# Kernel tuning notes

Hardware: AMD Instinct MI355X
Metric: run time of the kernel (lower is better)

Reference implementation:

```python
import jax, jax.numpy as jnp
import numpy as np

N = 8192
IN_DIM = 512
OUT_DIM = 256
ALPHA = 0.2  # LeakyReLU negative slope


def setup_inputs() -> dict:
    key = jax.random.key(0)
    k_nodes, k_edge, k_W, k_Wb, k_a1, k_a1b, k_a2, k_a2b = jax.random.split(key, 8)
    nodes = jax.random.normal(k_nodes, (N, IN_DIM), dtype=jnp.float32)
    edge_mat = jax.random.uniform(k_edge, (N, N)) > 0.5
    edge_mat = edge_mat | jnp.eye(N, dtype=bool)
    s_W = 1.0 / np.sqrt(IN_DIM)
    s_a = 1.0 / np.sqrt(OUT_DIM)
    W_w = jax.random.uniform(k_W, (OUT_DIM, IN_DIM), minval=-s_W, maxval=s_W, dtype=jnp.float32)
    W_b = jax.random.uniform(k_Wb, (OUT_DIM,), minval=-s_W, maxval=s_W, dtype=jnp.float32)
    a1_w = jax.random.uniform(k_a1, (1, OUT_DIM), minval=-s_a, maxval=s_a, dtype=jnp.float32)
    a1_b = jax.random.uniform(k_a1b, (1,), minval=-s_a, maxval=s_a, dtype=jnp.float32)
    a2_w = jax.random.uniform(k_a2, (1, OUT_DIM), minval=-s_a, maxval=s_a, dtype=jnp.float32)
    a2_b = jax.random.uniform(k_a2b, (1,), minval=-s_a, maxval=s_a, dtype=jnp.float32)
    return {"nodes": nodes, "edge_mat": edge_mat, "W_w": W_w, "W_b": W_b,
            "a1_w": a1_w, "a1_b": a1_b, "a2_w": a2_w, "a2_b": a2_b}


def reference(nodes, edge_mat, W_w, W_b, a1_w, a1_b, a2_w, a2_b):
    Wh = nodes @ W_w.T + W_b                      # [N, OUT_DIM]
    Wh1 = Wh @ a1_w.T + a1_b                      # [N, 1]
    Wh2 = Wh @ a2_w.T + a2_b                      # [N, 1]
    scores = jax.nn.leaky_relu(Wh1 + Wh2.T, negative_slope=ALPHA)  # [N, N]
    masked = jnp.where(edge_mat, scores, -jnp.inf)
    attention = jax.nn.softmax(masked, axis=1)    # [N, N]
    return attention @ Wh                         # [N, OUT_DIM]
```

## Files before the change

kernel.cpp:

```cpp
#include <hip/hip_runtime.h>
#include <hip/hip_bf16.h>
#include <stdint.h>


#define NN 8192
#define IND 512
#define OUTD 256

typedef __attribute__((ext_vector_type(8))) short short8;
typedef __attribute__((ext_vector_type(4))) short short4v;
typedef __attribute__((ext_vector_type(4))) float f32x4;
typedef __attribute__((ext_vector_type(4))) int i32x4;

static __device__ __forceinline__ short f2bf(float f) {
  return __builtin_bit_cast(short, __float2bfloat16(f));
}

extern "C" __global__ __launch_bounds__(256) void k_convert_w(
    const float* __restrict__ W, short* __restrict__ W2) {
  const int t = blockIdx.x * 256 + threadIdx.x;
  const int row = t >> 6, kb = t & 63;
  const float* src = W + row * IND + kb * 8;
  f32x4 x0 = *(const f32x4*)src;
  f32x4 x1 = *(const f32x4*)(src + 4);
  short8 o;
  o[0] = f2bf(x0[0]); o[1] = f2bf(x0[1]); o[2] = f2bf(x0[2]); o[3] = f2bf(x0[3]);
  o[4] = f2bf(x1[0]); o[5] = f2bf(x1[1]); o[6] = f2bf(x1[2]); o[7] = f2bf(x1[3]);
  *(short8*)(W2 + (size_t)kb * 2048 + row * 8) = o;
}

extern "C" __global__ __launch_bounds__(128) void k_wh(
    const float* __restrict__ nodes, const short* __restrict__ W2,
    const float* __restrict__ Wb, const float* __restrict__ a1w,
    const float* __restrict__ a1b, const float* __restrict__ a2w,
    const float* __restrict__ a2b, short* __restrict__ WhL,
    float* __restrict__ s1, float* __restrict__ s2) {
  const int tid = threadIdx.x;
  const int wv = tid >> 6, lane = tid & 63, g = lane >> 4, m = lane & 15;
  const int rowbase = blockIdx.x * 32 + wv * 16;

  f32x4 acc[16];
#pragma unroll
  for (int nf = 0; nf < 16; ++nf) acc[nf] = (f32x4){0.f, 0.f, 0.f, 0.f};

  const float* arow = nodes + (size_t)(rowbase + m) * IND;
  const short* bb = W2 + (size_t)g * 2048 + m * 8;
#pragma unroll 4
  for (int k0 = 0; k0 < IND; k0 += 32) {
    const float* ap = arow + k0 + g * 8;
    f32x4 x0 = *(const f32x4*)ap;
    f32x4 x1 = *(const f32x4*)(ap + 4);
    short8 af;
    af[0] = f2bf(x0[0]); af[1] = f2bf(x0[1]); af[2] = f2bf(x0[2]); af[3] = f2bf(x0[3]);
    af[4] = f2bf(x1[0]); af[5] = f2bf(x1[1]); af[6] = f2bf(x1[2]); af[7] = f2bf(x1[3]);
    const short* bk = bb + (size_t)(k0 >> 3) * 2048;
#pragma unroll
    for (int nf = 0; nf < 16; ++nf) {
      short8 bf = *(const short8*)(bk + nf * 128);
      acc[nf] = __builtin_amdgcn_mfma_f32_16x16x32_bf16(af, bf, acc[nf], 0, 0, 0);
    }
  }

  float p1[4] = {0.f, 0.f, 0.f, 0.f}, p2[4] = {0.f, 0.f, 0.f, 0.f};
#pragma unroll
  for (int nf = 0; nf < 16; ++nf) {
    const int n = nf * 16 + m;
    const float b = Wb[n], c1 = a1w[n], c2 = a2w[n];
#pragma unroll
    for (int r = 0; r < 4; ++r) {
      float v = acc[nf][r] + b;
      acc[nf][r] = v;
      p1[r] += c1 * v;
      p2[r] += c2 * v;
    }
  }
#pragma unroll
  for (int off = 1; off < 16; off <<= 1) {
#pragma unroll
    for (int r = 0; r < 4; ++r) {
      p1[r] += __shfl_xor(p1[r], off);
      p2[r] += __shfl_xor(p2[r], off);
    }
  }
  if (m == 0) {
    const float b1 = a1b[0], b2 = a2b[0];
#pragma unroll
    for (int r = 0; r < 4; ++r) {
      const int row = rowbase + g * 4 + r;
      s1[row] = p1[r] + b1;
      s2[row] = p2[r] + b2;
    }
  }

  const size_t cbase = ((size_t)(rowbase >> 3) + (g >> 1)) * 2048 + (g & 1) * 4;
#pragma unroll
  for (int nf = 0; nf < 16; ++nf) {
    short4v o;
#pragma unroll
    for (int r = 0; r < 4; ++r) o[r] = f2bf(acc[nf][r]);
    *(short4v*)(WhL + cbase + (size_t)(nf * 16 + m) * 8) = o;
  }
}

extern "C" __global__ __launch_bounds__(512, 2) void k_attn(
    const int* __restrict__ mask, const short* __restrict__ WhL,
    const float* __restrict__ s1, const float* __restrict__ s2,
    float* __restrict__ out) {
  __shared__ f32x4 cbuf[3][64][32];
  __shared__ float denl[8][32];

  const int tid = threadIdx.x;
  const int w = tid >> 6, lane = tid & 63, g = lane >> 4, m = lane & 15;
  const int rg = blockIdx.x * 32;

  const float s1a = s1[rg + m];
  const float s1b = s1[rg + 16 + m];

  f32x4 acc0[16], acc1[16];
#pragma unroll
  for (int nf = 0; nf < 16; ++nf) {
    acc0[nf] = (f32x4){0.f, 0.f, 0.f, 0.f};
    acc1[nf] = (f32x4){0.f, 0.f, 0.f, 0.f};
  }
  float den0 = 0.f, den1 = 0.f;

  const int* mr0 = mask + (size_t)(rg + m) * NN + w * 1024 + g * 8;
  const int* mr1 = mr0 + (size_t)16 * NN;
  const float* sp = s2 + w * 1024 + g * 8;
  const short* bb = WhL + ((size_t)w * 128 + g) * 2048 + (size_t)m * 8;

  i32x4 ca0 = __builtin_nontemporal_load((const i32x4*)mr0);
  i32x4 ca1 = __builtin_nontemporal_load((const i32x4*)(mr0 + 4));
  i32x4 cb0 = __builtin_nontemporal_load((const i32x4*)mr1);
  i32x4 cb1 = __builtin_nontemporal_load((const i32x4*)(mr1 + 4));
  f32x4 cs0 = *(const f32x4*)sp;
  f32x4 cs1 = *(const f32x4*)(sp + 4);

  auto build = [&](float s1h, const i32x4& xlo, const i32x4& xhi,
                   const f32x4& slo, const f32x4& shi, float& den) -> short8 {
    short8 af;
#pragma unroll
    for (int i = 0; i < 4; ++i) {
      float sv = s1h + slo[i];
      sv = fmaxf(sv, 0.2f * sv);
      float pv = (xlo[i] != 0) ? __expf(sv) : 0.f;
      den += pv;
      af[i] = f2bf(pv);
    }
#pragma unroll
    for (int i = 0; i < 4; ++i) {
      float sv = s1h + shi[i];
      sv = fmaxf(sv, 0.2f * sv);
      float pv = (xhi[i] != 0) ? __expf(sv) : 0.f;
      den += pv;
      af[i + 4] = f2bf(pv);
    }
    return af;
  };

#pragma unroll 2
  for (int u = 0; u < 32; ++u) {
    const int un = (u < 31) ? (u + 1) : 31;
    i32x4 na0 = __builtin_nontemporal_load((const i32x4*)(mr0 + un * 32));
    i32x4 na1 = __builtin_nontemporal_load((const i32x4*)(mr0 + un * 32 + 4));
    i32x4 nb0 = __builtin_nontemporal_load((const i32x4*)(mr1 + un * 32));
    i32x4 nb1 = __builtin_nontemporal_load((const i32x4*)(mr1 + un * 32 + 4));
    f32x4 ns0 = *(const f32x4*)(sp + un * 32);
    f32x4 ns1 = *(const f32x4*)(sp + un * 32 + 4);

    short8 af0 = build(s1a, ca0, ca1, cs0, cs1, den0);
    short8 af1 = build(s1b, cb0, cb1, cs0, cs1, den1);

    const short* bu = bb + (size_t)u * 8192;
#pragma unroll
    for (int nf = 0; nf < 16; ++nf) {
      short8 bf = *(const short8*)(bu + nf * 128);
      acc0[nf] = __builtin_amdgcn_mfma_f32_16x16x32_bf16(af0, bf, acc0[nf], 0, 0, 0);
      acc1[nf] = __builtin_amdgcn_mfma_f32_16x16x32_bf16(af1, bf, acc1[nf], 0, 0, 0);
    }
    ca0 = na0; ca1 = na1; cb0 = nb0; cb1 = nb1; cs0 = ns0; cs1 = ns1;
  }

  den0 += __shfl_xor(den0, 16); den0 += __shfl_xor(den0, 32);
  den1 += __shfl_xor(den1, 16); den1 += __shfl_xor(den1, 32);
  if (lane < 16) { denl[w][m] = den0; denl[w][16 + m] = den1; }

  auto storeacc = [&](int b) {
#pragma unroll
    for (int nf = 0; nf < 16; ++nf) {
      cbuf[b][lane][nf ^ (lane & 7)] = acc0[nf];
      cbuf[b][lane][(16 + nf) ^ (lane & 7)] = acc1[nf];
    }
  };
  auto addacc = [&](int b) {
#pragma unroll
    for (int nf = 0; nf < 16; ++nf) {
      acc0[nf] += cbuf[b][lane][nf ^ (lane & 7)];
      acc1[nf] += cbuf[b][lane][(16 + nf) ^ (lane & 7)];
    }
  };

  __syncthreads();
  if (w >= 4 && w <= 6) storeacc(w - 4);
  __syncthreads();
  if (w < 3) addacc(w);
  __syncthreads();
  if (w == 7) storeacc(0);
  if (w == 3) storeacc(1);
  __syncthreads();
  if (w == 0) addacc(0);
  if (w == 1) addacc(1);
  __syncthreads();
  if (w == 1) storeacc(0);
  if (w == 2) storeacc(1);
  __syncthreads();
  if (w == 0) {
    addacc(0);
    addacc(1);
    float d0 = 0.f, d1 = 0.f;
#pragma unroll
    for (int ww = 0; ww < 8; ++ww) { d0 += denl[ww][m]; d1 += denl[ww][16 + m]; }
#pragma unroll
    for (int r = 0; r < 4; ++r) {
      const int q = g * 4 + r;
      const float i0 = 1.f / __shfl(d0, q);
      const float i1 = 1.f / __shfl(d1, q);
#pragma unroll
      for (int nf = 0; nf < 16; ++nf) {
        out[(size_t)(rg + q) * OUTD + nf * 16 + m] = acc0[nf][r] * i0;
        out[(size_t)(rg + 16 + q) * OUTD + nf * 16 + m] = acc1[nf][r] * i1;
      }
    }
  }
}

extern "C" void kernel_launch(void* const* d_in, const int* in_sizes, int n_in,
                              void* d_out, int out_size, void* d_ws, size_t ws_size,
                              hipStream_t stream) {
  const float* nodes = (const float*)d_in[0];
  const int*   mask  = (const int*)d_in[1];
  const float* W_w   = (const float*)d_in[2];
  const float* W_b   = (const float*)d_in[3];
  const float* a1w   = (const float*)d_in[4];
  const float* a1b   = (const float*)d_in[5];
  const float* a2w   = (const float*)d_in[6];
  const float* a2b   = (const float*)d_in[7];
  float* out = (float*)d_out;

  char* ws = (char*)d_ws;
  short* WhL = (short*)(ws);
  float* s1  = (float*)(ws + (size_t)4 * 1024 * 1024);
  float* s2  = (float*)(ws + (size_t)4 * 1024 * 1024 + 32768);
  short* W2  = (short*)(ws + (size_t)4 * 1024 * 1024 + 65536);

  hipLaunchKernelGGL(k_convert_w, dim3(64), dim3(256), 0, stream, W_w, W2);
  hipLaunchKernelGGL(k_wh, dim3(256), dim3(128), 0, stream,
                     nodes, W2, W_b, a1w, a1b, a2w, a2b, WhL, s1, s2);
  hipLaunchKernelGGL(k_attn, dim3(256), dim3(512), 0, stream,
                     mask, WhL, s1, s2, out);
}
```

Baseline: 178.0 us.

## Pack mask into bitmap and split attention over key chunks with combine pass

Adds a pre-pass that packs the int32 adjacency mask into a bitmap with wave ballots, so the attention kernel reads bits instead of full ints. The attention kernel is restructured so each block covers 128 rows and a quarter of the key range. Each wave holds 32 rows and 1024 keys, and two waves reduce per row group. Partial numerators and denominators go to workspace, and a new combine kernel sums them and normalizes. This raises per-block WhL reuse and cuts the cross-wave reduction, at the cost of two extra launches and an extra 32 MB partial write and read.

```diff
diff --git a/kernel.cpp b/kernel.cpp
--- a/kernel.cpp
+++ b/kernel.cpp
@@ -10,7 +10,6 @@
 typedef __attribute__((ext_vector_type(8))) short short8;
 typedef __attribute__((ext_vector_type(4))) short short4v;
 typedef __attribute__((ext_vector_type(4))) float f32x4;
-typedef __attribute__((ext_vector_type(4))) int i32x4;
 
 static __device__ __forceinline__ short f2bf(float f) {
   return __builtin_bit_cast(short, __float2bfloat16(f));
@@ -102,19 +101,44 @@
   }
 }
 
+extern "C" __global__ __launch_bounds__(256) void k_mask(
+    const int* __restrict__ mask, uint32_t* __restrict__ bm) {
+  const int tid = threadIdx.x;
+  const int wv = tid >> 6, lane = tid & 63;
+  const int gw = blockIdx.x * 4 + wv;
+  const size_t base = (size_t)gw * 16384;
+#pragma unroll 4
+  for (int it = 0; it < 64; ++it) {
+    const size_t ib = base + (size_t)it * 256;
+    unsigned long long b0 = __ballot(mask[ib + lane] != 0);
+    unsigned long long b1 = __ballot(mask[ib + 64 + lane] != 0);
+    unsigned long long b2 = __ballot(mask[ib + 128 + lane] != 0);
+    unsigned long long b3 = __ballot(mask[ib + 192 + lane] != 0);
+    if (lane < 8) {
+      unsigned long long s01 = (lane & 2) ? b1 : b0;
+      unsigned long long s23 = (lane & 2) ? b3 : b2;
+      unsigned long long sel = (lane & 4) ? s23 : s01;
+      bm[ib / 32 + lane] = (uint32_t)(sel >> ((lane & 1) * 32));
+    }
+  }
+}
+
 extern "C" __global__ __launch_bounds__(512, 2) void k_attn(
-    const int* __restrict__ mask, const short* __restrict__ WhL,
+    const uint32_t* __restrict__ bm, const short* __restrict__ WhL,
     const float* __restrict__ s1, const float* __restrict__ s2,
-    float* __restrict__ out) {
-  __shared__ f32x4 cbuf[3][64][32];
-  __shared__ float denl[8][32];
+    float* __restrict__ pnum, float* __restrict__ pden) {
+  __shared__ f32x4 cbuf[4][64][16];
+  __shared__ float dbuf[4][2][16];
 
   const int tid = threadIdx.x;
   const int w = tid >> 6, lane = tid & 63, g = lane >> 4, m = lane & 15;
-  const int rg = blockIdx.x * 32;
-
-  const float s1a = s1[rg + m];
-  const float s1b = s1[rg + 16 + m];
+  const int rt = blockIdx.x >> 2, jc = blockIdx.x & 3;
+  const int rg = w >> 1, js = w & 1;
+  const int rowbase = rt * 128 + rg * 32;
+  const int jbase = jc * 2048 + js * 1024;
+
+  const float s1a = s1[rowbase + m];
+  const float s1b = s1[rowbase + 16 + m];
 
   f32x4 acc0[16], acc1[16];
 #pragma unroll
@@ -124,36 +148,25 @@
   }
   float den0 = 0.f, den1 = 0.f;
 
-  const int* mr0 = mask + (size_t)(rg + m) * NN + w * 1024 + g * 8;
-  const int* mr1 = mr0 + (size_t)16 * NN;
-  const float* sp = s2 + w * 1024 + g * 8;
-  const short* bb = WhL + ((size_t)w * 128 + g) * 2048 + (size_t)m * 8;
-
-  i32x4 ca0 = __builtin_nontemporal_load((const i32x4*)mr0);
-  i32x4 ca1 = __builtin_nontemporal_load((const i32x4*)(mr0 + 4));
-  i32x4 cb0 = __builtin_nontemporal_load((const i32x4*)mr1);
-  i32x4 cb1 = __builtin_nontemporal_load((const i32x4*)(mr1 + 4));
+  const uint32_t* bw0 = bm + (size_t)(rowbase + m) * 256 + (jbase >> 5);
+  const uint32_t* bw1 = bw0 + (size_t)16 * 256;
+  const float* sp = s2 + jbase + g * 8;
+  const short* bb = WhL + ((size_t)(jbase >> 3) + g) * 2048 + (size_t)m * 8;
+
+  uint32_t cw0 = bw0[0], cw1 = bw1[0];
   f32x4 cs0 = *(const f32x4*)sp;
   f32x4 cs1 = *(const f32x4*)(sp + 4);
 
-  auto build = [&](float s1h, const i32x4& xlo, const i32x4& xhi,
-                   const f32x4& slo, const f32x4& shi, float& den) -> short8 {
+  auto build = [&](float s1h, uint32_t bits, const f32x4& slo, const f32x4& shi,
+                   float& den) -> short8 {
     short8 af;
 #pragma unroll
-    for (int i = 0; i < 4; ++i) {
-      float sv = s1h + slo[i];
+    for (int i = 0; i < 8; ++i) {
+      float sv = s1h + (i < 4 ? slo[i] : shi[i - 4]);
       sv = fmaxf(sv, 0.2f * sv);
-      float pv = (xlo[i] != 0) ? __expf(sv) : 0.f;
+      float pv = (bits & (1u << i)) ? __expf(sv) : 0.f;
       den += pv;
       af[i] = f2bf(pv);
-    }
-#pragma unroll
-    for (int i = 0; i < 4; ++i) {
-      float sv = s1h + shi[i];
-      sv = fmaxf(sv, 0.2f * sv);
-      float pv = (xhi[i] != 0) ? __expf(sv) : 0.f;
-      den += pv;
-      af[i + 4] = f2bf(pv);
     }
     return af;
   };
@@ -161,15 +174,12 @@
 #pragma unroll 2
   for (int u = 0; u < 32; ++u) {
     const int un = (u < 31) ? (u + 1) : 31;
-    i32x4 na0 = __builtin_nontemporal_load((const i32x4*)(mr0 + un * 32));
-    i32x4 na1 = __builtin_nontemporal_load((const i32x4*)(mr0 + un * 32 + 4));
-    i32x4 nb0 = __builtin_nontemporal_load((const i32x4*)(mr1 + un * 32));
-    i32x4 nb1 = __builtin_nontemporal_load((const i32x4*)(mr1 + un * 32 + 4));
+    uint32_t nw0 = bw0[un], nw1 = bw1[un];
     f32x4 ns0 = *(const f32x4*)(sp + un * 32);
     f32x4 ns1 = *(const f32x4*)(sp + un * 32 + 4);
 
-    short8 af0 = build(s1a, ca0, ca1, cs0, cs1, den0);
-    short8 af1 = build(s1b, cb0, cb1, cs0, cs1, den1);
+    short8 af0 = build(s1a, cw0 >> (g * 8), cs0, cs1, den0);
+    short8 af1 = build(s1b, cw1 >> (g * 8), cs0, cs1, den1);
 
     const short* bu = bb + (size_t)u * 8192;
 #pragma unroll
@@ -178,60 +188,70 @@
       acc0[nf] = __builtin_amdgcn_mfma_f32_16x16x32_bf16(af0, bf, acc0[nf], 0, 0, 0);
       acc1[nf] = __builtin_amdgcn_mfma_f32_16x16x32_bf16(af1, bf, acc1[nf], 0, 0, 0);
     }
-    ca0 = na0; ca1 = na1; cb0 = nb0; cb1 = nb1; cs0 = ns0; cs1 = ns1;
+    cw0 = nw0; cw1 = nw1; cs0 = ns0; cs1 = ns1;
   }
 
   den0 += __shfl_xor(den0, 16); den0 += __shfl_xor(den0, 32);
   den1 += __shfl_xor(den1, 16); den1 += __shfl_xor(den1, 32);
-  if (lane < 16) { denl[w][m] = den0; denl[w][16 + m] = den1; }
-
-  auto storeacc = [&](int b) {
+
+  __syncthreads();
+  if (js) {
+#pragma unroll
+    for (int nf = 0; nf < 16; ++nf) cbuf[rg][lane][nf ^ (lane & 7)] = acc0[nf];
+    if (lane < 16) { dbuf[rg][0][m] = den0; dbuf[rg][1][m] = den1; }
+  }
+  __syncthreads();
+  if (!js) {
+#pragma unroll
+    for (int nf = 0; nf < 16; ++nf) acc0[nf] += cbuf[rg][lane][nf ^ (lane & 7)];
+    den0 += dbuf[rg][0][m];
+    den1 += dbuf[rg][1][m];
+  }
+  __syncthreads();
+  if (js) {
+#pragma unroll
+    for (int nf = 0; nf < 16; ++nf) cbuf[rg][lane][nf ^ (lane & 7)] = acc1[nf];
+  }
+  __syncthreads();
+  if (js) return;
+
+#pragma unroll
+  for (int nf = 0; nf < 16; ++nf) acc1[nf] += cbuf[rg][lane][nf ^ (lane & 7)];
+
+  if (lane < 16) {
+    pden[jc * NN + rowbase + m] = den0;
+    pden[jc * NN + rowbase + 16 + m] = den1;
+  }
+
+  float* pn = pnum + (size_t)jc * NN * OUTD;
+#pragma unroll
+  for (int r = 0; r < 4; ++r) {
+    const int q = g * 4 + r;
+    const size_t r0 = (size_t)(rowbase + q) * OUTD;
+    const size_t r1 = (size_t)(rowbase + 16 + q) * OUTD;
 #pragma unroll
     for (int nf = 0; nf < 16; ++nf) {
-      cbuf[b][lane][nf ^ (lane & 7)] = acc0[nf];
-      cbuf[b][lane][(16 + nf) ^ (lane & 7)] = acc1[nf];
-    }
-  };
-  auto addacc = [&](int b) {
-#pragma unroll
-    for (int nf = 0; nf < 16; ++nf) {
-      acc0[nf] += cbuf[b][lane][nf ^ (lane & 7)];
-      acc1[nf] += cbuf[b][lane][(16 + nf) ^ (lane & 7)];
-    }
-  };
-
-  __syncthreads();
-  if (w >= 4 && w <= 6) storeacc(w - 4);
-  __syncthreads();
-  if (w < 3) addacc(w);
-  __syncthreads();
-  if (w == 7) storeacc(0);
-  if (w == 3) storeacc(1);
-  __syncthreads();
-  if (w == 0) addacc(0);
-  if (w == 1) addacc(1);
-  __syncthreads();
-  if (w == 1) storeacc(0);
-  if (w == 2) storeacc(1);
-  __syncthreads();
-  if (w == 0) {
-    addacc(0);
-    addacc(1);
-    float d0 = 0.f, d1 = 0.f;
-#pragma unroll
-    for (int ww = 0; ww < 8; ++ww) { d0 += denl[ww][m]; d1 += denl[ww][16 + m]; }
-#pragma unroll
-    for (int r = 0; r < 4; ++r) {
-      const int q = g * 4 + r;
-      const float i0 = 1.f / __shfl(d0, q);
-      const float i1 = 1.f / __shfl(d1, q);
-#pragma unroll
-      for (int nf = 0; nf < 16; ++nf) {
-        out[(size_t)(rg + q) * OUTD + nf * 16 + m] = acc0[nf][r] * i0;
-        out[(size_t)(rg + 16 + q) * OUTD + nf * 16 + m] = acc1[nf][r] * i1;
-      }
-    }
-  }
+      pn[r0 + nf * 16 + m] = acc0[nf][r];
+      pn[r1 + nf * 16 + m] = acc1[nf][r];
+    }
+  }
+}
+
+extern "C" __global__ __launch_bounds__(256) void k_comb(
+    const float* __restrict__ pnum, const float* __restrict__ pden,
+    float* __restrict__ out) {
+  const int idx = blockIdx.x * 256 + threadIdx.x;
+  const int row = idx >> 6, c4 = (idx & 63) * 4;
+  f32x4 s = (f32x4){0.f, 0.f, 0.f, 0.f};
+  float d = 0.f;
+#pragma unroll
+  for (int jc = 0; jc < 4; ++jc) {
+    f32x4 v = *(const f32x4*)(pnum + ((size_t)jc * NN + row) * OUTD + c4);
+    s += v;
+    d += pden[jc * NN + row];
+  }
+  const float inv = 1.f / d;
+  *(f32x4*)(out + (size_t)row * OUTD + c4) = s * inv;
 }
 
 extern "C" void kernel_launch(void* const* d_in, const int* in_sizes, int n_in,
@@ -248,14 +268,20 @@
   float* out = (float*)d_out;
 
   char* ws = (char*)d_ws;
-  short* WhL = (short*)(ws);
-  float* s1  = (float*)(ws + (size_t)4 * 1024 * 1024);
-  float* s2  = (float*)(ws + (size_t)4 * 1024 * 1024 + 32768);
-  short* W2  = (short*)(ws + (size_t)4 * 1024 * 1024 + 65536);
+  short*    WhL  = (short*)(ws);
+  float*    s1   = (float*)(ws + (size_t)4  * 1024 * 1024);
+  float*    s2   = (float*)(ws + (size_t)4  * 1024 * 1024 + 32768);
+  short*    W2   = (short*)(ws + (size_t)4  * 1024 * 1024 + 65536);
+  uint32_t* bmp  = (uint32_t*)(ws + (size_t)5  * 1024 * 1024);
+  float*    pnum = (float*)(ws + (size_t)16 * 1024 * 1024);
+  float*    pden = (float*)(ws + (size_t)48 * 1024 * 1024);
 
   hipLaunchKernelGGL(k_convert_w, dim3(64), dim3(256), 0, stream, W_w, W2);
   hipLaunchKernelGGL(k_wh, dim3(256), dim3(128), 0, stream,
                      nodes, W2, W_b, a1w, a1b, a2w, a2b, WhL, s1, s2);
+  hipLaunchKernelGGL(k_mask, dim3(1024), dim3(256), 0, stream, mask, bmp);
   hipLaunchKernelGGL(k_attn, dim3(256), dim3(512), 0, stream,
-                     mask, WhL, s1, s2, out);
-}
+                     bmp, WhL, s1, s2, pnum, pden);
+  hipLaunchKernelGGL(k_comb, dim3(2048), dim3(256), 0, stream,
+                     pnum, pden, out);
+}
```

New measurement: 281.4 us. +58.1%, slower.
